# Optimization experiments

Measured on AMD Instinct MI355X. Metric: run time of the kernel, lower is better.

Reference implementation:

```python
import jax, jax.numpy as jnp
import numpy as np
from jax import lax

L, B, H, Z, V = 64, 32, 256, 256, 32000  # steps, max_ast_depth, hidden=units, latent, vocab


def setup_inputs() -> dict:
    key = jax.random.key(0)
    ks = jax.random.split(key, 32)
    p = lambda i, shape: jax.random.normal(ks[i], shape, dtype=jnp.float32) * 0.05
    inp = {
        "nodes": jax.random.randint(ks[0], (L, B), 0, V),
        "edges": jax.random.randint(ks[1], (L, B), 0, 2) > 0,
        "enc_init": jax.random.normal(ks[2], (B, H), dtype=jnp.float32) * 0.001,
        "eps": jax.random.normal(ks[3], (B, Z), dtype=jnp.float32),
        "emb": p(4, (V, H)),
    }
    for j, n in enumerate(["enc_c", "enc_s", "dec_c", "dec_s"]):
        inp[n + "_Wih"] = p(5 + 4 * j, (3 * H, H))
        inp[n + "_Whh"] = p(6 + 4 * j, (3 * H, H))
        inp[n + "_bih"] = p(7 + 4 * j, (3 * H,))
        inp[n + "_bhh"] = p(8 + 4 * j, (3 * H,))
    inp["W_mean"] = p(21, (Z, H)); inp["b_mean"] = p(22, (Z,))
    inp["W_logv"] = p(23, (Z, H)); inp["b_logv"] = p(24, (Z,))
    inp["W_l2h"] = p(25, (H, Z)); inp["b_l2h"] = p(26, (H,))
    inp["W_voc"] = p(27, (V, H)); inp["b_voc"] = p(28, (V,))
    return inp


def _gru_cell(Wih, Whh, bih, bhh, x, h):
    # torch.nn.GRU single-layer cell; x, h: [B, H]
    gi = x @ Wih.T + bih
    gh = h @ Whh.T + bhh
    ir, iz, inn = jnp.split(gi, 3, axis=-1)
    hr, hz, hn = jnp.split(gh, 3, axis=-1)
    r = jax.nn.sigmoid(ir + hr)
    zg = jax.nn.sigmoid(iz + hz)
    n = jnp.tanh(inn + r * hn)
    return (1.0 - zg) * n + zg * h


def _tree_rnn(pc, ps, emb_nodes, edges, h0):
    # emb_nodes: [L, B, H], edges: [L, B] bool, h0: [B, H]
    # each step runs child & sibling GRUs on the SAME state, selects per node by edge
    def step(h, xe):
        x, e = xe
        hc = _gru_cell(*pc, x, h)
        hs = _gru_cell(*ps, x, h)
        h_new = jnp.where(e[:, None], hc, hs)
        return h_new, h_new  # 1-layer GRU, seq_len 1: output == new state
    h_final, outs = lax.scan(step, h0, (emb_nodes, edges))
    return outs, h_final  # outs: [L, B, H]


def reference(nodes, edges, enc_init, eps, emb,
              enc_c_Wih, enc_c_Whh, enc_c_bih, enc_c_bhh,
              enc_s_Wih, enc_s_Whh, enc_s_bih, enc_s_bhh,
              dec_c_Wih, dec_c_Whh, dec_c_bih, dec_c_bhh,
              dec_s_Wih, dec_s_Whh, dec_s_bih, dec_s_bhh,
              W_mean, b_mean, W_logv, b_logv, W_l2h, b_l2h, W_voc, b_voc):
    x = emb[nodes]  # [L, B, H]
    _, h_enc = _tree_rnn((enc_c_Wih, enc_c_Whh, enc_c_bih, enc_c_bhh),
                         (enc_s_Wih, enc_s_Whh, enc_s_bih, enc_s_bhh),
                         x, edges, enc_init)
    mean = h_enc @ W_mean.T + b_mean          # [B, Z]
    logv = h_enc @ W_logv.T + b_logv
    z = eps * jnp.exp(0.5 * logv) + mean      # reparameterization
    h0 = z @ W_l2h.T + b_l2h                  # decoder initial state [B, H]
    outs, _ = _tree_rnn((dec_c_Wih, dec_c_Whh, dec_c_bih, dec_c_bhh),
                        (dec_s_Wih, dec_s_Whh, dec_s_bih, dec_s_bhh),
                        x, edges, h0)         # [L, B, H]
    logits = outs @ W_voc.T + b_voc           # [L, B, V]
    logp = jax.nn.log_softmax(logits, axis=-1)
    return logp, mean, logv, z
```

## Files before the change

kernel.cpp:

```cpp
#include <hip/hip_runtime.h>
#include <stdint.h>

typedef unsigned short u16;
typedef unsigned int u32;

#define L_STEPS 64
#define B_SZ 32
#define H_SZ 256
#define Z_SZ 256
#define V_SZ 32000
#define H2 128
#define G3H 768

typedef _Float16 h2_t __attribute__((ext_vector_type(2)));
typedef _Float16 f16x8 __attribute__((ext_vector_type(8)));
typedef float f32x4 __attribute__((ext_vector_type(4)));

#define WHH2_OFF   0
#define WIH2_OFF   393216
#define WM2_OFF    786432
#define WLV2_OFF   819200
#define WL2H2_OFF  851968
#define GI2_OFF    884736
#define OUTS2_OFF  4030464
#define W16_OFF    4292608
#define WS_NEEDED  ((size_t)(W16_OFF + 4096000) * 4)

#define NPART 20

#define OUT_MEAN_OFF  65536000
#define OUT_LOGV_OFF  65544192
#define OUT_Z_OFF     65552384

__device__ __forceinline__ float fdot2(h2_t a, h2_t b, float c){
#if __has_builtin(__builtin_amdgcn_fdot2)
  return __builtin_amdgcn_fdot2(a, b, c, false);
#else
  return c + (float)a.x*(float)b.x + (float)a.y*(float)b.y;
#endif
}
__device__ __forceinline__ float sigm(float x){ return 1.f/(1.f + __expf(-x)); }

struct PackTArgs { const float2* src[11]; int n_h2[11]; int dstoff[11]; };

__global__ __launch_bounds__(256) void k_packt(PackTArgs p, h2_t* wsh){
  int m = blockIdx.y;
  int r = blockIdx.x*256 + threadIdx.x;
  if (r >= p.n_h2[m]) return;
  int row = r >> 7, k2 = r & 127;
  float2 f = p.src[m][r];
  h2_t h; h.x = (_Float16)f.x; h.y = (_Float16)f.y;
  int off = (((row>>6)*32 + (k2>>2))*64 + (row&63))*4 + (k2&3);
  wsh[p.dstoff[m] + off] = h;
}

__global__ __launch_bounds__(256) void k_packv(const float2* __restrict__ src,
                                               h2_t* __restrict__ dst, int total){
  int idx = blockIdx.x*256 + threadIdx.x;
  if (idx >= total) return;
  float2 f = src[idx];
  h2_t h; h.x = (_Float16)f.x; h.y = (_Float16)f.y;
  dst[idx] = h;
}

struct GiArgs { const float* bih[4]; };

__global__ __launch_bounds__(256) void k_gi(const int* __restrict__ nodes,
                                            const float* __restrict__ emb,
                                            const h2_t* __restrict__ wih2,
                                            GiArgs ga, h2_t* __restrict__ gi2){
  int l = blockIdx.x, g = blockIdx.y, t = threadIdx.x;
  __shared__ __align__(16) h2_t x2[B_SZ*132];
  #pragma unroll
  for (int it=0; it<16; ++it){
    int lin = it*256 + t;
    int bb = lin >> 7, k2 = lin & 127;
    int node = nodes[l*B_SZ + bb];
    float2 f = ((const float2*)(emb + (size_t)node*H_SZ))[k2];
    h2_t r; r.x=(_Float16)f.x; r.y=(_Float16)f.y;
    x2[bb*132 + k2] = r;
  }
  __syncthreads();
  const float* bih = ga.bih[g];
  for (int jc=0; jc<3; ++jc){
    int j = jc*256 + t;
    float acc[32];
    #pragma unroll
    for (int bb=0;bb<32;bb++) acc[bb]=0.f;
    const float4* Wv = (const float4*)wih2 + (size_t)g*24576 + (j>>6)*2048 + (j&63);
    #pragma unroll 2
    for (int kb=0;kb<32;kb++){
      union{float4 f; h2_t h[4];} w4;
      w4.f = Wv[kb*64];
      #pragma unroll
      for (int kc=0;kc<4;kc++){
        h2_t w = w4.h[kc];
        int k2 = kb*4 + kc;
        #pragma unroll
        for (int bb=0;bb<32;bb++) acc[bb] = fdot2(x2[bb*132+k2], w, acc[bb]);
      }
    }
    float bvv = bih[j];
    int base = (g*2048 + l*B_SZ)*384 + (j>>1);
    #pragma unroll
    for (int bb=0;bb<32;bb++){
      float own = acc[bb] + bvv;
      float oth = __shfl_xor(own, 1, 64);
      if (!(t&1)){
        h2_t r; r.x=(_Float16)own; r.y=(_Float16)oth;
        gi2[base + bb*384] = r;
      }
    }
  }
}

struct ScanArgs {
  const float* bhh[4];
  const float* b_mean; const float* b_logv; const float* b_l2h;
  const float* enc_init; const float* eps;
};

__global__ __launch_bounds__(768) void k_scan(const int* __restrict__ edges, ScanArgs sa,
                                              const h2_t* __restrict__ wsh,
                                              h2_t* __restrict__ outs2,
                                              float* __restrict__ out){
  int b = blockIdx.x, t = threadIdx.x;
  int i = t & 255, gate = t >> 8;
  int lane = t & 63, rb = t >> 6;
  __shared__ float h_lds[H_SZ];
  __shared__ __align__(16) h2_t hs2[H2];
  __shared__ float g_lds[512];
  __shared__ float s_bhh[4*G3H];
  __shared__ int s_edge[L_STEPS];
  const _Float16* gi_all = (const _Float16*)(wsh + GI2_OFF);

  if (t < H_SZ) h_lds[t] = sa.enc_init[b*H_SZ + t];
  if (t < L_STEPS) s_edge[t] = edges[t*B_SZ + b];
  #pragma unroll
  for (int m=0;m<4;m++) s_bhh[m*G3H + t] = sa.bhh[m][t];
  __syncthreads();
  if (t < H2){ h2_t r; r.x=(_Float16)h_lds[2*t]; r.y=(_Float16)h_lds[2*t+1]; hs2[t]=r; }
  __syncthreads();

  const float4* hsv = (const float4*)hs2;

  for (int ph=0; ph<2; ++ph){
    for (int l=0; l<L_STEPS; ++l){
      int e = s_edge[l];
      int gsel = (ph ? 2 : 0) + (e ? 0 : 1);
      float gi0=0.f, gi1=0.f, gi2v=0.f;
      if (t < H_SZ){
        const _Float16* gr = gi_all + (size_t)(gsel*2048 + l*B_SZ + b)*G3H;
        gi0  = (float)gr[i];
        gi1  = (float)gr[256+i];
        gi2v = (float)gr[512+i];
      }
      float bv = s_bhh[gsel*G3H + t];
      const float4* Wv = (const float4*)wsh + (size_t)gsel*24576 + rb*2048 + lane;
      float a0=0.f,a1=0.f,a2=0.f,a3=0.f;
      float4 wa[8], wb[8];
      #pragma unroll
      for (int j=0;j<8;j++) wa[j] = Wv[j*64];
      #pragma unroll
      for (int c=0;c<4;c++){
        float4* cur = (c&1)? wb : wa;
        float4* nxt = (c&1)? wa : wb;
        if (c<3){
          const float4* Wn = Wv + (size_t)(c+1)*512;
          #pragma unroll
          for (int j=0;j<8;j++) nxt[j] = Wn[j*64];
        }
        #pragma unroll
        for (int j=0;j<8;j++){
          union{float4 f; h2_t h[4];} w, x;
          w.f = cur[j];
          x.f = hsv[c*8+j];
          a0 = fdot2(x.h[0], w.h[0], a0);
          a1 = fdot2(x.h[1], w.h[1], a1);
          a2 = fdot2(x.h[2], w.h[2], a2);
          a3 = fdot2(x.h[3], w.h[3], a3);
        }
      }
      float acc = (a0+a1)+(a2+a3) + bv;
      if (gate) g_lds[(gate-1)*256 + i] = acc;
      __syncthreads();
      if (t < H_SZ){
        float r = sigm(gi0 + acc);
        float z = sigm(gi1 + g_lds[i]);
        float n = tanhf(gi2v + r*g_lds[256+i]);
        float hn = (1.f - z)*n + z*h_lds[i];
        h_lds[i] = hn;
        float ho = __shfl_xor(hn, 1, 64);
        if (!(i & 1)){
          h2_t pk; pk.x=(_Float16)hn; pk.y=(_Float16)ho;
          hs2[i>>1] = pk;
          if (ph) outs2[(l*B_SZ + b)*H2 + (i>>1)] = pk;
        }
      }
      __syncthreads();
    }

    if (ph == 0){
      if (t < H_SZ){
        const float4* WmV = (const float4*)(wsh + WM2_OFF)  + (t>>6)*2048 + (t&63);
        const float4* WlV = (const float4*)(wsh + WLV2_OFF) + (t>>6)*2048 + (t&63);
        float m0=0.f,m1=0.f,m2=0.f,m3=0.f, l0=0.f,l1=0.f,l2=0.f,l3=0.f;
        #pragma unroll 8
        for (int kb=0;kb<32;kb++){
          union{float4 f; h2_t h[4];} wm, wl, x;
          x.f  = hsv[kb];
          wm.f = WmV[kb*64];
          wl.f = WlV[kb*64];
          m0=fdot2(x.h[0],wm.h[0],m0); m1=fdot2(x.h[1],wm.h[1],m1);
          m2=fdot2(x.h[2],wm.h[2],m2); m3=fdot2(x.h[3],wm.h[3],m3);
          l0=fdot2(x.h[0],wl.h[0],l0); l1=fdot2(x.h[1],wl.h[1],l1);
          l2=fdot2(x.h[2],wl.h[2],l2); l3=fdot2(x.h[3],wl.h[3],l3);
        }
        float am = (m0+m1)+(m2+m3) + sa.b_mean[t];
        float al = (l0+l1)+(l2+l3) + sa.b_logv[t];
        float zv = sa.eps[b*Z_SZ + t] * __expf(0.5f*al) + am;
        out[OUT_MEAN_OFF + b*Z_SZ + t] = am;
        out[OUT_LOGV_OFF + b*Z_SZ + t] = al;
        out[OUT_Z_OFF    + b*Z_SZ + t] = zv;
        h_lds[t] = zv;
      }
      __syncthreads();
      if (t < H2){ h2_t r; r.x=(_Float16)h_lds[2*t]; r.y=(_Float16)h_lds[2*t+1]; hs2[t]=r; }
      __syncthreads();
      float h0v = 0.f;
      if (t < H_SZ){
        const float4* WzV = (const float4*)(wsh + WL2H2_OFF) + (t>>6)*2048 + (t&63);
        float z0=0.f,z1=0.f,z2=0.f,z3=0.f;
        #pragma unroll 8
        for (int kb=0;kb<32;kb++){
          union{float4 f; h2_t h[4];} w, x;
          x.f = hsv[kb];
          w.f = WzV[kb*64];
          z0=fdot2(x.h[0],w.h[0],z0); z1=fdot2(x.h[1],w.h[1],z1);
          z2=fdot2(x.h[2],w.h[2],z2); z3=fdot2(x.h[3],w.h[3],z3);
        }
        h0v = (z0+z1)+(z2+z3) + sa.b_l2h[t];
      }
      __syncthreads();
      if (t < H_SZ) h_lds[t] = h0v;
      __syncthreads();
      if (t < H2){ h2_t r; r.x=(_Float16)h_lds[2*t]; r.y=(_Float16)h_lds[2*t+1]; hs2[t]=r; }
      __syncthreads();
    }
  }
}

__global__ __launch_bounds__(256) void k_lse(const h2_t* __restrict__ outs2,
                                             const _Float16* __restrict__ wv16,
                                             const float* __restrict__ bvoc,
                                             float* __restrict__ part){
  int t = threadIdx.x;
  int lane = t & 63, w = t >> 6;
  int wm = w & 1, wn = w >> 1;
  int Mb = blockIdx.x * 64, ns = blockIdx.y;
  int lr = lane & 15, lq = lane >> 4;

  __shared__ __align__(16) float4 As4[4*64*8];

  #pragma unroll
  for (int q=0;q<8;q++){
    int c = q*256 + t;
    int kc = c >> 9, row = (c >> 3) & 63, kb = c & 7;
    float4 d = ((const float4*)(outs2 + (size_t)(Mb+row)*H2))[kc*8 + kb];
    As4[kc*512 + row*8 + (kb ^ (row & 7))] = d;
  }
  __syncthreads();

  union{float4 f; f16x8 h;} af[4][2][2];
  #pragma unroll
  for (int kc=0;kc<4;kc++)
    #pragma unroll
    for (int mi=0;mi<2;mi++)
      #pragma unroll
      for (int kk=0;kk<2;kk++){
        int row = wm*32 + mi*16 + lr;
        af[kc][mi][kk].f = As4[kc*512 + row*8 + ((kk*4+lq) ^ (row&7))];
      }

  float mrun[2][4], srun[2][4];
  #pragma unroll
  for (int mi=0;mi<2;mi++)
    #pragma unroll
    for (int rg=0;rg<4;rg++){ mrun[mi][rg] = -1e30f; srun[mi][rg] = 0.f; }

  for (int nb=0; nb<25; ++nb){
    int col0 = ns*3200 + nb*128 + wn*64;
    f32x4 acc[2][4];
    #pragma unroll
    for (int mi=0;mi<2;mi++)
      #pragma unroll
      for (int nj=0;nj<4;nj++) acc[mi][nj] = (f32x4){0.f,0.f,0.f,0.f};

    float bias[4];
    #pragma unroll
    for (int nj=0;nj<4;nj++){
      int col = col0 + nj*16 + lr;
      bias[nj] = bvoc[col];
      const float4* bp = (const float4*)(wv16 + (size_t)col*H_SZ);
      #pragma unroll
      for (int kc=0;kc<4;kc++)
        #pragma unroll
        for (int kk=0;kk<2;kk++){
          union{float4 f; f16x8 h;} bf;
          bf.f = bp[kc*8 + kk*4 + lq];
          #pragma unroll
          for (int mi=0;mi<2;mi++)
            acc[mi][nj] = __builtin_amdgcn_mfma_f32_16x16x32_f16(
                            af[kc][mi][kk].h, bf.h, acc[mi][nj], 0, 0, 0);
        }
    }
    #pragma unroll
    for (int mi=0;mi<2;mi++)
      #pragma unroll
      for (int rg=0;rg<4;rg++){
        float v0 = acc[mi][0][rg] + bias[0];
        float v1 = acc[mi][1][rg] + bias[1];
        float v2 = acc[mi][2][rg] + bias[2];
        float v3 = acc[mi][3][rg] + bias[3];
        float mx = fmaxf(fmaxf(v0,v1), fmaxf(v2,v3));
        #pragma unroll
        for (int o=1;o<16;o<<=1) mx = fmaxf(mx, __shfl_xor(mx, o, 64));
        float sv = __expf(v0-mx)+__expf(v1-mx)+__expf(v2-mx)+__expf(v3-mx);
        #pragma unroll
        for (int o=1;o<16;o<<=1) sv += __shfl_xor(sv, o, 64);
        float nm = fmaxf(mrun[mi][rg], mx);
        srun[mi][rg] = srun[mi][rg]*__expf(mrun[mi][rg]-nm) + sv*__expf(mx-nm);
        mrun[mi][rg] = nm;
      }
  }

  if (lr == 0){
    #pragma unroll
    for (int mi=0;mi<2;mi++)
      #pragma unroll
      for (int rg=0;rg<4;rg++){
        int row = Mb + wm*32 + mi*16 + lq*4 + rg;
        int p = ns*2 + wn;
        part[(row*NPART + p)*2 + 0] = mrun[mi][rg];
        part[(row*NPART + p)*2 + 1] = srun[mi][rg];
      }
  }
}

__global__ __launch_bounds__(256) void k_lsered(const float* __restrict__ part,
                                                float* __restrict__ lse){
  int r = blockIdx.x*256 + threadIdx.x;
  if (r >= 2048) return;
  float M = -1e30f;
  #pragma unroll
  for (int p=0;p<NPART;p++) M = fmaxf(M, part[(r*NPART+p)*2]);
  float S = 0.f;
  #pragma unroll
  for (int p=0;p<NPART;p++) S += part[(r*NPART+p)*2+1] * __expf(part[(r*NPART+p)*2] - M);
  lse[r] = M + logf(S);
}

__global__ __launch_bounds__(256) void k_gemm3(const h2_t* __restrict__ outs2,
                                               const _Float16* __restrict__ wv16,
                                               const float* __restrict__ bvoc,
                                               const float* __restrict__ lse,
                                               float* __restrict__ outf){
  int t = threadIdx.x;
  int lane = t & 63, w = t >> 6;
  int wm = w & 1, wn = w >> 1;
  int Mb = blockIdx.x * 64, Nb = blockIdx.y * 128;
  int lr = lane & 15, lq = lane >> 4;

  __shared__ __align__(16) _Float16 As[64*64];
  __shared__ __align__(16) _Float16 Bs[128*64];

  f32x4 acc[2][4];
  #pragma unroll
  for (int mi=0;mi<2;mi++)
    #pragma unroll
    for (int nj=0;nj<4;nj++) acc[mi][nj] = (f32x4){0.f,0.f,0.f,0.f};

  for (int kc=0; kc<4; ++kc){
    #pragma unroll
    for (int q=0;q<2;q++){
      int ch = q*256 + t;
      int row = ch >> 3, kb = ch & 7;
      float4 d = ((const float4*)(outs2 + (size_t)(Mb + row)*H2 + kc*32))[kb];
      ((float4*)As)[row*8 + (kb ^ (row & 7))] = d;
    }
    #pragma unroll
    for (int q=0;q<4;q++){
      int ch = q*256 + t;
      int row = ch >> 3, kb = ch & 7;
      float4 d = ((const float4*)(wv16 + (size_t)(Nb + row)*H_SZ + kc*64))[kb];
      ((float4*)Bs)[row*8 + (kb ^ (row & 7))] = d;
    }
    __syncthreads();
    union{float4 f; f16x8 h;} af[2][2], bf[4][2];
    #pragma unroll
    for (int mi=0;mi<2;mi++)
      #pragma unroll
      for (int kk=0;kk<2;kk++){
        int row = wm*32 + mi*16 + lr;
        int ks = kk*4 + lq;
        af[mi][kk].f = ((const float4*)As)[row*8 + (ks ^ (row & 7))];
      }
    #pragma unroll
    for (int nj=0;nj<4;nj++)
      #pragma unroll
      for (int kk=0;kk<2;kk++){
        int row = wn*64 + nj*16 + lr;
        int ks = kk*4 + lq;
        bf[nj][kk].f = ((const float4*)Bs)[row*8 + (ks ^ (row & 7))];
      }
    #pragma unroll
    for (int kk=0;kk<2;kk++)
      #pragma unroll
      for (int mi=0;mi<2;mi++)
        #pragma unroll
        for (int nj=0;nj<4;nj++)
          acc[mi][nj] = __builtin_amdgcn_mfma_f32_16x16x32_f16(
                          af[mi][kk].h, bf[nj][kk].h, acc[mi][nj], 0, 0, 0);
    __syncthreads();
  }

  #pragma unroll
  for (int mi=0;mi<2;mi++){
    int r0 = Mb + wm*32 + mi*16 + lq*4;
    float lsev[4];
    #pragma unroll
    for (int rg=0;rg<4;rg++) lsev[rg] = lse[r0+rg];
    #pragma unroll
    for (int nj=0;nj<4;nj++){
      int col = Nb + wn*64 + nj*16 + lr;
      float bias = bvoc[col];
      #pragma unroll
      for (int rg=0;rg<4;rg++)
        outf[(size_t)(r0 + rg)*V_SZ + col] = acc[mi][nj][rg] + bias - lsev[rg];
    }
  }
}

__global__ __launch_bounds__(512) void k_gemm(const h2_t* __restrict__ outs2,
                                              const float* __restrict__ wv,
                                              const float* __restrict__ bvoc,
                                              float* __restrict__ outf){
  int t = threadIdx.x;
  int vq = t & 31, rq = t >> 5;
  int Nb = blockIdx.x * 256, Mb = blockIdx.y * 128;
  __shared__ __align__(16) h2_t A[16*128];
  __shared__ __align__(16) h2_t Bss[16*256];
  float acc[8][8];
  #pragma unroll
  for (int a=0;a<8;a++){
    #pragma unroll
    for (int c=0;c<8;c++) acc[a][c]=0.f;
  }

  for (int kc=0;kc<8;kc++){
    {
      int r = t >> 2, q = t & 3;
      union{float4 f; h2_t h[4];} u;
      u.f = ((const float4*)(outs2 + (Mb + r)*H2 + kc*16))[q];
      #pragma unroll
      for (int uu=0; uu<4; ++uu) A[(q*4+uu)*128 + r] = u.h[uu];
    }
    {
      int v = t >> 1, q = t & 1;
      const float* wrow = wv + (size_t)(Nb + v)*H_SZ + kc*32 + q*16;
      #pragma unroll
      for (int p=0;p<4;p++){
        float4 f = ((const float4*)wrow)[p];
        h2_t h0; h0.x=(_Float16)f.x; h0.y=(_Float16)f.y;
        h2_t h1; h1.x=(_Float16)f.z; h1.y=(_Float16)f.w;
        Bss[(q*8+p*2  )*256 + v] = h0;
        Bss[(q*8+p*2+1)*256 + v] = h1;
      }
    }
    __syncthreads();
    #pragma unroll 2
    for (int k2=0;k2<16;k2++){
      union{float4 f; h2_t h[4];} a0, a1, b0, b1;
      a0.f = *(const float4*)(A  + k2*128 + rq*8);
      a1.f = *(const float4*)(A  + k2*128 + rq*8 + 4);
      b0.f = *(const float4*)(Bss + k2*256 + vq*4);
      b1.f = *(const float4*)(Bss + k2*256 + vq*4 + 128);
      #pragma unroll
      for (int ii=0;ii<8;ii++){
        h2_t av = (ii<4)? a0.h[ii] : a1.h[ii-4];
        #pragma unroll
        for (int jj=0;jj<8;jj++){
          h2_t bv = (jj<4)? b0.h[jj] : b1.h[jj-4];
          acc[ii][jj] = fdot2(av, bv, acc[ii][jj]);
        }
      }
    }
    __syncthreads();
  }

  float bias0[4], bias1[4];
  #pragma unroll
  for (int jj=0;jj<4;jj++){
    bias0[jj] = bvoc[Nb + 4*vq + jj];
    bias1[jj] = bvoc[Nb + 128 + 4*vq + jj];
  }
  #pragma unroll
  for (int ii=0;ii<8;ii++){
    size_t base = (size_t)(Mb + rq*8 + ii)*(size_t)V_SZ + (size_t)Nb;
    float4 o0, o1;
    o0.x = acc[ii][0]+bias0[0]; o0.y = acc[ii][1]+bias0[1];
    o0.z = acc[ii][2]+bias0[2]; o0.w = acc[ii][3]+bias0[3];
    o1.x = acc[ii][4]+bias1[0]; o1.y = acc[ii][5]+bias1[1];
    o1.z = acc[ii][6]+bias1[2]; o1.w = acc[ii][7]+bias1[3];
    *(float4*)(outf + base + 4*vq)       = o0;
    *(float4*)(outf + base + 128 + 4*vq) = o1;
  }
}

__global__ __launch_bounds__(256) void k_softmax(float* __restrict__ outf){
  int rrow = blockIdx.x, t = threadIdx.x;
  float4* row = (float4*)(outf + (size_t)rrow * V_SZ);
  float4 v[32];
  #pragma unroll
  for (int i=0;i<31;i++) v[i] = row[i*256 + t];
  if (t < 64) v[31] = row[7936 + t];
  else { v[31].x = -1e30f; v[31].y = -1e30f; v[31].z = -1e30f; v[31].w = -1e30f; }

  float m = -1e30f;
  #pragma unroll
  for (int i=0;i<32;i++) m = fmaxf(m, fmaxf(fmaxf(v[i].x, v[i].y), fmaxf(v[i].z, v[i].w)));

  __shared__ float sred[4];
  __shared__ float sbc;
  int wid = t >> 6, lane = t & 63;
  #pragma unroll
  for (int o=32;o;o>>=1) m = fmaxf(m, __shfl_xor(m, o, 64));
  if (lane==0) sred[wid] = m;
  __syncthreads();
  if (t==0) sbc = fmaxf(fmaxf(sred[0],sred[1]), fmaxf(sred[2],sred[3]));
  __syncthreads();
  m = sbc;
  __syncthreads();

  float s = 0.f;
  #pragma unroll
  for (int i=0;i<32;i++){
    s += __expf(v[i].x - m) + __expf(v[i].y - m) + __expf(v[i].z - m) + __expf(v[i].w - m);
  }
  #pragma unroll
  for (int o=32;o;o>>=1) s += __shfl_xor(s, o, 64);
  if (lane==0) sred[wid] = s;
  __syncthreads();
  if (t==0) sbc = sred[0]+sred[1]+sred[2]+sred[3];
  __syncthreads();
  float lse = m + logf(sbc);

  #pragma unroll
  for (int i=0;i<31;i++){
    v[i].x -= lse; v[i].y -= lse; v[i].z -= lse; v[i].w -= lse;
    row[i*256 + t] = v[i];
  }
  if (t < 64){
    v[31].x -= lse; v[31].y -= lse; v[31].z -= lse; v[31].w -= lse;
    row[7936 + t] = v[31];
  }
}

extern "C" void kernel_launch(void* const* d_in, const int* in_sizes, int n_in,
                              void* d_out, int out_size, void* d_ws, size_t ws_size,
                              hipStream_t stream){
  const int* nodes = (const int*)d_in[0];
  const int* edges = (const int*)d_in[1];
  h2_t* wsh = (h2_t*)d_ws;
  float* outf = (float*)d_out;
  bool mfma_path = (ws_size >= WS_NEEDED);

  PackTArgs pt;
  const int srcidx[11] = {6,10,14,18, 5,9,13,17, 21,23,25};
  for (int k=0;k<11;k++){
    pt.src[k] = (const float2*)d_in[srcidx[k]];
    pt.n_h2[k] = (k < 8) ? 98304 : 32768;
  }
  for (int k=0;k<4;k++) pt.dstoff[k]   = WHH2_OFF + k*98304;
  for (int k=0;k<4;k++) pt.dstoff[4+k] = WIH2_OFF + k*98304;
  pt.dstoff[8] = WM2_OFF; pt.dstoff[9] = WLV2_OFF; pt.dstoff[10] = WL2H2_OFF;
  k_packt<<<dim3(384,11), dim3(256), 0, stream>>>(pt, wsh);

  if (mfma_path)
    k_packv<<<dim3(16000), dim3(256), 0, stream>>>((const float2*)d_in[27],
                                                   wsh + W16_OFF, 4096000);

  GiArgs ga;
  ga.bih[0]=(const float*)d_in[7];  ga.bih[1]=(const float*)d_in[11];
  ga.bih[2]=(const float*)d_in[15]; ga.bih[3]=(const float*)d_in[19];
  k_gi<<<dim3(64,4), dim3(256), 0, stream>>>(nodes, (const float*)d_in[4], wsh + WIH2_OFF, ga, wsh + GI2_OFF);

  ScanArgs sa;
  sa.bhh[0]=(const float*)d_in[8];  sa.bhh[1]=(const float*)d_in[12];
  sa.bhh[2]=(const float*)d_in[16]; sa.bhh[3]=(const float*)d_in[20];
  sa.b_mean=(const float*)d_in[22]; sa.b_logv=(const float*)d_in[24]; sa.b_l2h=(const float*)d_in[26];
  sa.enc_init=(const float*)d_in[2]; sa.eps=(const float*)d_in[3];
  k_scan<<<dim3(32), dim3(768), 0, stream>>>(edges, sa, wsh, wsh + OUTS2_OFF, outf);

  if (mfma_path){
    float* part = (float*)(wsh + GI2_OFF);
    float* lse  = part + 2048*NPART*2;
    k_lse<<<dim3(32,10), dim3(256), 0, stream>>>(wsh + OUTS2_OFF,
                                                 (const _Float16*)(wsh + W16_OFF),
                                                 (const float*)d_in[28], part);
    k_lsered<<<dim3(8), dim3(256), 0, stream>>>(part, lse);
    k_gemm3<<<dim3(32,250), dim3(256), 0, stream>>>(wsh + OUTS2_OFF,
                                                    (const _Float16*)(wsh + W16_OFF),
                                                    (const float*)d_in[28], lse, outf);
  } else {
    k_gemm<<<dim3(125,16), dim3(512), 0, stream>>>(wsh + OUTS2_OFF, (const float*)d_in[27],
                                                   (const float*)d_in[28], outf);
    k_softmax<<<dim3(2048), dim3(256), 0, stream>>>(outf);
  }
}
```

Measured before the change: 1.160 ms.

## Retile vocab LSE pass into many blocks and prefetch next-step GRU weights

The log-sum-exp partial kernel now gives each block one 64x128 logits tile, staged through swizzled LDS, and does a block-level reduction. It launches 8000 blocks instead of 320 blocks that each looped over 25 column tiles, and the partial count per row grows to 250. In the serial GRU scan, the first slice of the next step's recurrent weights is prefetched into registers before the current step finishes. The remaining weight loads are now issued in a simple unrolled loop instead of the double-buffered scheme. The trade-offs are more partial-reduction work and extra LDS staging, while the scan may lose some of the latency hiding it had before.

After: 1.084 ms. 1.07x faster.

```diff
diff --git a/kernel.cpp b/kernel.cpp
--- a/kernel.cpp
+++ b/kernel.cpp
@@ -26,7 +26,7 @@
 #define W16_OFF    4292608
 #define WS_NEEDED  ((size_t)(W16_OFF + 4096000) * 4)
 
-#define NPART 20
+#define NPART 250
 
 #define OUT_MEAN_OFF  65536000
 #define OUT_LOGV_OFF  65544192
@@ -144,6 +144,14 @@
 
   const float4* hsv = (const float4*)hs2;
 
+  float4 pf[8];
+  {
+    int gsel0 = s_edge[0] ? 0 : 1;
+    const float4* W0 = (const float4*)wsh + (size_t)gsel0*24576 + rb*2048 + lane;
+    #pragma unroll
+    for (int j=0;j<8;j++) pf[j] = W0[j*64];
+  }
+
   for (int ph=0; ph<2; ++ph){
     for (int l=0; l<L_STEPS; ++l){
       int e = s_edge[l];
@@ -158,27 +166,34 @@
       float bv = s_bhh[gsel*G3H + t];
       const float4* Wv = (const float4*)wsh + (size_t)gsel*24576 + rb*2048 + lane;
       float a0=0.f,a1=0.f,a2=0.f,a3=0.f;
-      float4 wa[8], wb[8];
-      #pragma unroll
-      for (int j=0;j<8;j++) wa[j] = Wv[j*64];
-      #pragma unroll
-      for (int c=0;c<4;c++){
-        float4* cur = (c&1)? wb : wa;
-        float4* nxt = (c&1)? wa : wb;
-        if (c<3){
-          const float4* Wn = Wv + (size_t)(c+1)*512;
+      #pragma unroll
+      for (int j=0;j<8;j++){
+        union{float4 f; h2_t h[4];} w, x;
+        w.f = pf[j];
+        x.f = hsv[j];
+        a0 = fdot2(x.h[0], w.h[0], a0);
+        a1 = fdot2(x.h[1], w.h[1], a1);
+        a2 = fdot2(x.h[2], w.h[2], a2);
+        a3 = fdot2(x.h[3], w.h[3], a3);
+      }
+      #pragma unroll 8
+      for (int kb=8;kb<32;kb++){
+        union{float4 f; h2_t h[4];} w, x;
+        w.f = Wv[kb*64];
+        x.f = hsv[kb];
+        a0 = fdot2(x.h[0], w.h[0], a0);
+        a1 = fdot2(x.h[1], w.h[1], a1);
+        a2 = fdot2(x.h[2], w.h[2], a2);
+        a3 = fdot2(x.h[3], w.h[3], a3);
+      }
+      {
+        int gsel_n = -1;
+        if (l < L_STEPS-1)      gsel_n = (ph ? 2 : 0) + (s_edge[l+1] ? 0 : 1);
+        else if (ph == 0)       gsel_n = 2 + (s_edge[0] ? 0 : 1);
+        if (gsel_n >= 0){
+          const float4* Wn = (const float4*)wsh + (size_t)gsel_n*24576 + rb*2048 + lane;
           #pragma unroll
-          for (int j=0;j<8;j++) nxt[j] = Wn[j*64];
-        }
-        #pragma unroll
-        for (int j=0;j<8;j++){
-          union{float4 f; h2_t h[4];} w, x;
-          w.f = cur[j];
-          x.f = hsv[c*8+j];
-          a0 = fdot2(x.h[0], w.h[0], a0);
-          a1 = fdot2(x.h[1], w.h[1], a1);
-          a2 = fdot2(x.h[2], w.h[2], a2);
-          a3 = fdot2(x.h[3], w.h[3], a3);
+          for (int j=0;j<8;j++) pf[j] = Wn[j*64];
         }
       }
       float acc = (a0+a1)+(a2+a3) + bv;
@@ -257,93 +272,95 @@
   int t = threadIdx.x;
   int lane = t & 63, w = t >> 6;
   int wm = w & 1, wn = w >> 1;
-  int Mb = blockIdx.x * 64, ns = blockIdx.y;
+  int Mb = blockIdx.x * 64, Nb = blockIdx.y * 128;
   int lr = lane & 15, lq = lane >> 4;
 
-  __shared__ __align__(16) float4 As4[4*64*8];
-
-  #pragma unroll
-  for (int q=0;q<8;q++){
-    int c = q*256 + t;
-    int kc = c >> 9, row = (c >> 3) & 63, kb = c & 7;
-    float4 d = ((const float4*)(outs2 + (size_t)(Mb+row)*H2))[kc*8 + kb];
-    As4[kc*512 + row*8 + (kb ^ (row & 7))] = d;
-  }
-  __syncthreads();
-
-  union{float4 f; f16x8 h;} af[4][2][2];
-  #pragma unroll
-  for (int kc=0;kc<4;kc++)
+  __shared__ __align__(16) _Float16 As[64*64];
+  __shared__ __align__(16) _Float16 Bs[128*64];
+  __shared__ float red[2][64][2];
+
+  f32x4 acc[2][4];
+  #pragma unroll
+  for (int mi=0;mi<2;mi++)
+    #pragma unroll
+    for (int nj=0;nj<4;nj++) acc[mi][nj] = (f32x4){0.f,0.f,0.f,0.f};
+
+  for (int kc=0; kc<4; ++kc){
+    #pragma unroll
+    for (int q=0;q<2;q++){
+      int ch = q*256 + t;
+      int row = ch >> 3, kb = ch & 7;
+      float4 d = ((const float4*)(outs2 + (size_t)(Mb + row)*H2 + kc*32))[kb];
+      ((float4*)As)[row*8 + (kb ^ (row & 7))] = d;
+    }
+    #pragma unroll
+    for (int q=0;q<4;q++){
+      int ch = q*256 + t;
+      int row = ch >> 3, kb = ch & 7;
+      float4 d = ((const float4*)(wv16 + (size_t)(Nb + row)*H_SZ + kc*64))[kb];
+      ((float4*)Bs)[row*8 + (kb ^ (row & 7))] = d;
+    }
+    __syncthreads();
+    union{float4 f; f16x8 h;} af[2][2], bf[4][2];
     #pragma unroll
     for (int mi=0;mi<2;mi++)
       #pragma unroll
       for (int kk=0;kk<2;kk++){
         int row = wm*32 + mi*16 + lr;
-        af[kc][mi][kk].f = As4[kc*512 + row*8 + ((kk*4+lq) ^ (row&7))];
-      }
-
-  float mrun[2][4], srun[2][4];
+        int ks = kk*4 + lq;
+        af[mi][kk].f = ((const float4*)As)[row*8 + (ks ^ (row & 7))];
+      }
+    #pragma unroll
+    for (int nj=0;nj<4;nj++)
+      #pragma unroll
+      for (int kk=0;kk<2;kk++){
+        int row = wn*64 + nj*16 + lr;
+        int ks = kk*4 + lq;
+        bf[nj][kk].f = ((const float4*)Bs)[row*8 + (ks ^ (row & 7))];
+      }
+    #pragma unroll
+    for (int kk=0;kk<2;kk++)
+      #pragma unroll
+      for (int mi=0;mi<2;mi++)
+        #pragma unroll
+        for (int nj=0;nj<4;nj++)
+          acc[mi][nj] = __builtin_amdgcn_mfma_f32_16x16x32_f16(
+                          af[mi][kk].h, bf[nj][kk].h, acc[mi][nj], 0, 0, 0);
+    __syncthreads();
+  }
+
+  float bias[4];
+  #pragma unroll
+  for (int nj=0;nj<4;nj++) bias[nj] = bvoc[Nb + wn*64 + nj*16 + lr];
   #pragma unroll
   for (int mi=0;mi<2;mi++)
     #pragma unroll
-    for (int rg=0;rg<4;rg++){ mrun[mi][rg] = -1e30f; srun[mi][rg] = 0.f; }
-
-  for (int nb=0; nb<25; ++nb){
-    int col0 = ns*3200 + nb*128 + wn*64;
-    f32x4 acc[2][4];
-    #pragma unroll
-    for (int mi=0;mi<2;mi++)
-      #pragma unroll
-      for (int nj=0;nj<4;nj++) acc[mi][nj] = (f32x4){0.f,0.f,0.f,0.f};
-
-    float bias[4];
-    #pragma unroll
-    for (int nj=0;nj<4;nj++){
-      int col = col0 + nj*16 + lr;
-      bias[nj] = bvoc[col];
-      const float4* bp = (const float4*)(wv16 + (size_t)col*H_SZ);
-      #pragma unroll
-      for (int kc=0;kc<4;kc++)
-        #pragma unroll
-        for (int kk=0;kk<2;kk++){
-          union{float4 f; f16x8 h;} bf;
-          bf.f = bp[kc*8 + kk*4 + lq];
-          #pragma unroll
-          for (int mi=0;mi<2;mi++)
-            acc[mi][nj] = __builtin_amdgcn_mfma_f32_16x16x32_f16(
-                            af[kc][mi][kk].h, bf.h, acc[mi][nj], 0, 0, 0);
-        }
-    }
-    #pragma unroll
-    for (int mi=0;mi<2;mi++)
-      #pragma unroll
-      for (int rg=0;rg<4;rg++){
-        float v0 = acc[mi][0][rg] + bias[0];
-        float v1 = acc[mi][1][rg] + bias[1];
-        float v2 = acc[mi][2][rg] + bias[2];
-        float v3 = acc[mi][3][rg] + bias[3];
-        float mx = fmaxf(fmaxf(v0,v1), fmaxf(v2,v3));
-        #pragma unroll
-        for (int o=1;o<16;o<<=1) mx = fmaxf(mx, __shfl_xor(mx, o, 64));
-        float sv = __expf(v0-mx)+__expf(v1-mx)+__expf(v2-mx)+__expf(v3-mx);
-        #pragma unroll
-        for (int o=1;o<16;o<<=1) sv += __shfl_xor(sv, o, 64);
-        float nm = fmaxf(mrun[mi][rg], mx);
-        srun[mi][rg] = srun[mi][rg]*__expf(mrun[mi][rg]-nm) + sv*__expf(mx-nm);
-        mrun[mi][rg] = nm;
-      }
-  }
-
-  if (lr == 0){
-    #pragma unroll
-    for (int mi=0;mi<2;mi++)
-      #pragma unroll
-      for (int rg=0;rg<4;rg++){
-        int row = Mb + wm*32 + mi*16 + lq*4 + rg;
-        int p = ns*2 + wn;
-        part[(row*NPART + p)*2 + 0] = mrun[mi][rg];
-        part[(row*NPART + p)*2 + 1] = srun[mi][rg];
-      }
+    for (int rg=0;rg<4;rg++){
+      float v0 = acc[mi][0][rg] + bias[0];
+      float v1 = acc[mi][1][rg] + bias[1];
+      float v2 = acc[mi][2][rg] + bias[2];
+      float v3 = acc[mi][3][rg] + bias[3];
+      float mx = fmaxf(fmaxf(v0,v1), fmaxf(v2,v3));
+      #pragma unroll
+      for (int o=1;o<16;o<<=1) mx = fmaxf(mx, __shfl_xor(mx, o, 64));
+      float sv = __expf(v0-mx)+__expf(v1-mx)+__expf(v2-mx)+__expf(v3-mx);
+      #pragma unroll
+      for (int o=1;o<16;o<<=1) sv += __shfl_xor(sv, o, 64);
+      if (lr == 0){
+        int rloc = wm*32 + mi*16 + lq*4 + rg;
+        red[wn][rloc][0] = mx;
+        red[wn][rloc][1] = sv;
+      }
+    }
+  __syncthreads();
+  if (t < 64){
+    float m0 = red[0][t][0], s0 = red[0][t][1];
+    float m1 = red[1][t][0], s1 = red[1][t][1];
+    float M = fmaxf(m0, m1);
+    float S = s0*__expf(m0-M) + s1*__expf(m1-M);
+    int row = Mb + t;
+    part[((size_t)row*NPART + blockIdx.y)*2 + 0] = M;
+    part[((size_t)row*NPART + blockIdx.y)*2 + 1] = S;
   }
 }
 
@@ -351,12 +368,11 @@
                                                 float* __restrict__ lse){
   int r = blockIdx.x*256 + threadIdx.x;
   if (r >= 2048) return;
+  const float* pr = part + (size_t)r*NPART*2;
   float M = -1e30f;
-  #pragma unroll
-  for (int p=0;p<NPART;p++) M = fmaxf(M, part[(r*NPART+p)*2]);
+  for (int p=0;p<NPART;p++) M = fmaxf(M, pr[p*2]);
   float S = 0.f;
-  #pragma unroll
-  for (int p=0;p<NPART;p++) S += part[(r*NPART+p)*2+1] * __expf(part[(r*NPART+p)*2] - M);
+  for (int p=0;p<NPART;p++) S += pr[p*2+1] * __expf(pr[p*2] - M);
   lse[r] = M + logf(S);
 }
 
@@ -605,9 +621,9 @@
   if (mfma_path){
     float* part = (float*)(wsh + GI2_OFF);
     float* lse  = part + 2048*NPART*2;
-    k_lse<<<dim3(32,10), dim3(256), 0, stream>>>(wsh + OUTS2_OFF,
-                                                 (const _Float16*)(wsh + W16_OFF),
-                                                 (const float*)d_in[28], part);
+    k_lse<<<dim3(32,250), dim3(256), 0, stream>>>(wsh + OUTS2_OFF,
+                                                  (const _Float16*)(wsh + W16_OFF),
+                                                  (const float*)d_in[28], part);
     k_lsered<<<dim3(8), dim3(256), 0, stream>>>(part, lse);
     k_gemm3<<<dim3(32,250), dim3(256), 0, stream>>>(wsh + OUTS2_OFF,
                                                     (const _Float16*)(wsh + W16_OFF),
```
